# Performance work log

Hardware: AMD Instinct MI355X
Metric: run time of the kernel (lower is better)

The kernel has to match this reference:

```python
import jax, jax.numpy as jnp
import numpy as np

B, S, D, H = 4, 2048, 1024, 16
HD = D // H  # head_dim = 64


def setup_inputs() -> dict:
    key = jax.random.key(0)
    ks = jax.random.split(key, 9)
    sc = 1.0 / np.sqrt(D)
    return {
        "x": jax.random.normal(ks[0], (B, S, D), dtype=jnp.float32),
        "Wq": jax.random.normal(ks[1], (D, D), dtype=jnp.float32) * sc,
        "bq": jnp.zeros((D,), dtype=jnp.float32),
        "Wk": jax.random.normal(ks[2], (D, D), dtype=jnp.float32) * sc,
        "bk": jnp.zeros((D,), dtype=jnp.float32),
        "Wv": jax.random.normal(ks[3], (D, D), dtype=jnp.float32) * sc,
        "bv": jnp.zeros((D,), dtype=jnp.float32),
        "Wo": jax.random.normal(ks[4], (D, D), dtype=jnp.float32) * sc,
        "bo": jnp.zeros((D,), dtype=jnp.float32),
    }


def reference(x, Wq, bq, Wk, bk, Wv, bv, Wo, bo):
    # QKV projections (torch Linear: x @ W.T + b), reshape to [B, H, S, HD]
    def proj(W, b):
        return (x @ W.T + b).reshape(B, S, H, HD).transpose(0, 2, 1, 3)

    Q, K, V = proj(Wq, bq), proj(Wk, bk), proj(Wv, bv)
    scores = jnp.einsum("bhqd,bhkd->bhqk", Q, K) / jnp.sqrt(jnp.float32(HD))
    attn = jax.nn.softmax(scores, axis=-1)  # dropout is identity at eval
    ctx = jnp.einsum("bhqk,bhkd->bhqd", attn, V)
    ctx = ctx.transpose(0, 2, 1, 3).reshape(B, S, D)
    out = ctx @ Wo.T + bo
    return out, attn
```

## Files before the change

### kernel.cpp

```cpp
#include <hip/hip_runtime.h>
#include <stdint.h>

#define Mm 8192
#define Dd 1024

typedef unsigned short u16;
typedef __attribute__((ext_vector_type(8))) short bf16x8;
typedef __attribute__((ext_vector_type(4))) float f32x4;
typedef __attribute__((ext_vector_type(4))) u16 u16x4;

__device__ __forceinline__ u16 f2bf(float f) {
  union { float f; uint32_t u; } c; c.f = f;
  uint32_t u = c.u;
  return (u16)((u + 0x7fffu + ((u >> 16) & 1u)) >> 16);
}

__device__ __forceinline__ float EXP2(float x) {
#if __has_builtin(__builtin_amdgcn_exp2f)
  return __builtin_amdgcn_exp2f(x);
#else
  return exp2f(x);
#endif
}

__device__ __forceinline__ float LOG2(float x) {
#if __has_builtin(__builtin_amdgcn_logf)
  return __builtin_amdgcn_logf(x);
#else
  return log2f(x);
#endif
}

__device__ __forceinline__ uint32_t cvtpk(float a, float b) {
  uint32_t r;
  asm("v_cvt_pk_bf16_f32 %0, %1, %2" : "=v"(r) : "v"(a), "v"(b));
  return r;
}

__device__ __forceinline__ void gll16(const void* g, void* l) {
  __builtin_amdgcn_global_load_lds((const __attribute__((address_space(1))) void*)g,
                                   (__attribute__((address_space(3))) void*)l, 16, 0, 0);
}

__global__ void cvt_all(const float* __restrict__ x, const float* __restrict__ wq,
                        const float* __restrict__ wk, const float* __restrict__ wv,
                        const float* __restrict__ wo, u16* __restrict__ out) {
  const int xn4 = 2097152, wn4 = 262144;
  const int total = xn4 + 4 * wn4;
  int i = blockIdx.x * blockDim.x + threadIdx.x;
  int stride = gridDim.x * blockDim.x;
  for (; i < total; i += stride) {
    const float* src; int off;
    if (i < xn4) { src = x; off = i; }
    else {
      int j = i - xn4; int wsel = j >> 18; off = j & (wn4 - 1);
      src = (wsel == 0) ? wq : (wsel == 1) ? wk : (wsel == 2) ? wv : wo;
    }
    float4 v = ((const float4*)src)[off];
    u16x4 o;
    o.x = f2bf(v.x); o.y = f2bf(v.y); o.z = f2bf(v.z); o.w = f2bf(v.w);
    ((u16x4*)out)[i] = o;
  }
}

__global__ __launch_bounds__(256) void gemm_qkv(
    const u16* __restrict__ A, const u16* __restrict__ Wt,
    const float* __restrict__ bq, const float* __restrict__ bk, const float* __restrict__ bv,
    u16* __restrict__ Qo, u16* __restrict__ Ko, u16* __restrict__ Vo, float qscale)
{
  __shared__ u16 As[128 * 32];
  __shared__ u16 Bs[128 * 32];
  const int K = 1024, tiles_n = 24;
  int nwg = 64 * 24;
  int bid = blockIdx.x;
  { int q = nwg >> 3; bid = (bid & 7) * q + (bid >> 3); }
  int tm = bid / tiles_n, tn = bid % tiles_n;
  int tid = threadIdx.x;
  int wid = tid >> 6, lane = tid & 63;
  int wr = wid >> 1, wc = wid & 1;

  f32x4 acc[4][4] = {};
  int a_row = wr * 64 + (lane & 15);
  int b_row = wc * 64 + (lane & 15);
  int frag_k = (lane >> 4) * 8;

  const u16* ga0 = A + (size_t)(tm * 128 + wid * 32 + (lane >> 2)) * K + (lane & 3) * 8;
  const u16* ga1 = ga0 + (size_t)16 * K;
  const u16* gb0 = Wt + (size_t)(tn * 128 + wid * 32 + (lane >> 2)) * K + (lane & 3) * 8;
  const u16* gb1 = gb0 + (size_t)16 * K;
  u16* lA0 = As + wid * 1024;
  u16* lA1 = As + wid * 1024 + 512;
  u16* lB0 = Bs + wid * 1024;
  u16* lB1 = Bs + wid * 1024 + 512;

  for (int kt = 0; kt < K; kt += 32) {
    gll16(ga0 + kt, lA0);
    gll16(ga1 + kt, lA1);
    gll16(gb0 + kt, lB0);
    gll16(gb1 + kt, lB1);
    __syncthreads();
    bf16x8 af[4], bfr[4];
#pragma unroll
    for (int i = 0; i < 4; i++)
      af[i] = *(const bf16x8*)(As + (a_row + i * 16) * 32 + frag_k);
#pragma unroll
    for (int i = 0; i < 4; i++)
      bfr[i] = *(const bf16x8*)(Bs + (b_row + i * 16) * 32 + frag_k);
#pragma unroll
    for (int i = 0; i < 4; i++)
#pragma unroll
      for (int j = 0; j < 4; j++)
        acc[i][j] = __builtin_amdgcn_mfma_f32_16x16x32_bf16(af[i], bfr[j], acc[i][j], 0, 0, 0);
    __syncthreads();
  }

#pragma unroll
  for (int i = 0; i < 4; i++) {
#pragma unroll
    for (int j = 0; j < 4; j++) {
      int col = tn * 128 + wc * 64 + j * 16 + (lane & 15);
      int wsel = col >> 10, c10 = col & 1023;
      int h = c10 >> 6, hd = c10 & 63;
      float bvv = (wsel == 0 ? bq : wsel == 1 ? bk : bv)[c10];
      int row0 = tm * 128 + wr * 64 + i * 16 + (lane >> 4) * 4;
      int b_ = row0 >> 11, s0 = row0 & 2047;
      if (wsel == 2) {
        u16x4 o;
#pragma unroll
        for (int r = 0; r < 4; r++) o[r] = f2bf(acc[i][j][r] + bvv);
        *(u16x4*)&Vo[((size_t)(b_ * 16 + h) * 64 + hd) * 2048 + s0] = o;
      } else {
        u16* dst = (wsel == 0) ? Qo : Ko;
        float sc = (wsel == 0) ? qscale : 1.0f;
#pragma unroll
        for (int r = 0; r < 4; r++)
          dst[(((size_t)(b_ * 16 + h) * 2048 + (s0 + r)) << 6) + hd] = f2bf((acc[i][j][r] + bvv) * sc);
      }
    }
  }
}

__global__ __launch_bounds__(256) void gemm_out(
    const u16* __restrict__ A, const u16* __restrict__ Bt,
    const float* __restrict__ bias, float* __restrict__ out,
    int M, int N, int K)
{
  __shared__ u16 As[128 * 32];
  __shared__ u16 Bs[128 * 32];
  int tiles_n = N >> 7;
  int nwg = (M >> 7) * tiles_n;
  int bid = blockIdx.x;
  { int q = nwg >> 3; bid = (bid & 7) * q + (bid >> 3); }
  int tm = bid / tiles_n, tn = bid % tiles_n;
  int tid = threadIdx.x;
  int wid = tid >> 6, lane = tid & 63;
  int wr = wid >> 1, wc = wid & 1;

  f32x4 acc[4][4] = {};
  int a_row = wr * 64 + (lane & 15);
  int b_row = wc * 64 + (lane & 15);
  int frag_k = (lane >> 4) * 8;

  const u16* ga0 = A + (size_t)(tm * 128 + wid * 32 + (lane >> 2)) * K + (lane & 3) * 8;
  const u16* ga1 = ga0 + (size_t)16 * K;
  const u16* gb0 = Bt + (size_t)(tn * 128 + wid * 32 + (lane >> 2)) * K + (lane & 3) * 8;
  const u16* gb1 = gb0 + (size_t)16 * K;
  u16* lA0 = As + wid * 1024;
  u16* lA1 = As + wid * 1024 + 512;
  u16* lB0 = Bs + wid * 1024;
  u16* lB1 = Bs + wid * 1024 + 512;

  for (int kt = 0; kt < K; kt += 32) {
    gll16(ga0 + kt, lA0);
    gll16(ga1 + kt, lA1);
    gll16(gb0 + kt, lB0);
    gll16(gb1 + kt, lB1);
    __syncthreads();
    bf16x8 af[4], bfr[4];
#pragma unroll
    for (int i = 0; i < 4; i++)
      af[i] = *(const bf16x8*)(As + (a_row + i * 16) * 32 + frag_k);
#pragma unroll
    for (int i = 0; i < 4; i++)
      bfr[i] = *(const bf16x8*)(Bs + (b_row + i * 16) * 32 + frag_k);
#pragma unroll
    for (int i = 0; i < 4; i++)
#pragma unroll
      for (int j = 0; j < 4; j++)
        acc[i][j] = __builtin_amdgcn_mfma_f32_16x16x32_bf16(af[i], bfr[j], acc[i][j], 0, 0, 0);
    __syncthreads();
  }

#pragma unroll
  for (int i = 0; i < 4; i++)
#pragma unroll
    for (int j = 0; j < 4; j++) {
      int col = tn * 128 + wc * 64 + j * 16 + (lane & 15);
      float bv = bias[col];
#pragma unroll
      for (int r = 0; r < 4; r++) {
        int row = tm * 128 + wr * 64 + i * 16 + (lane >> 4) * 4 + r;
        out[(size_t)row * N + col] = acc[i][j][r] + bv;
      }
    }
}

__global__ __launch_bounds__(512, 4) void attn_fused2(
    const u16* __restrict__ Qb, const u16* __restrict__ Kb,
    const u16* __restrict__ Vtb, float* __restrict__ attn_out,
    u16* __restrict__ ctxb)
{
  __shared__ u16 Ks[4][4096];
  __shared__ u16 Vs[4][4096];
  __shared__ u16 Ps[8192];

  int bid = blockIdx.x;
  int swz = (bid & 7) * 64 + (bid >> 3);
  int bh = swz >> 3, qtb = swz & 7;
  int tid = threadIdx.x, w = tid >> 6, lane = tid & 63;
  int g = lane >> 4, l15 = lane & 15;

  const u16* Kg = Kb + (size_t)bh * 2048 * 64;
  const u16* Vg = Vtb + (size_t)bh * 64 * 2048;
  const u16* Qg0 = Qb + ((size_t)bh * 2048 + qtb * 256) * 64;
  const u16* Qg1 = Qg0 + (size_t)128 * 64;
  float* Ag0 = attn_out + ((size_t)bh * 2048 + qtb * 256) * 2048;
  float* Ag1 = Ag0 + (size_t)128 * 2048;

  int qloc = w * 16 + l15;
  bf16x8 aqA0 = *(const bf16x8*)(Qg0 + (size_t)qloc * 64 + g * 8);
  bf16x8 aqA1 = *(const bf16x8*)(Qg0 + (size_t)qloc * 64 + 32 + g * 8);
  bf16x8 aqB0 = *(const bf16x8*)(Qg1 + (size_t)qloc * 64 + g * 8);
  bf16x8 aqB1 = *(const bf16x8*)(Qg1 + (size_t)qloc * 64 + 32 + g * 8);

  int srow = w * 8 + (lane >> 3);
  int schunk = (lane & 7) ^ (lane >> 3);
  const u16* Ksrc = Kg + (size_t)srow * 64 + schunk * 8;
  const u16* Vsrc = Vg + (size_t)srow * 2048 + schunk * 8;

  int xq = (qloc & 7) << 4;
  char* Pb = (char*)Ps + qloc * 128;
  int b_ = bh >> 4, h = bh & 15;

  float ls0 = 0.f, ls1 = 0.f, ls2 = 0.f, ls3 = 0.f;
#pragma unroll
  for (int p = 0; p < 3; p++)
    gll16(Ksrc + (size_t)p * 4096, (char*)Ks[p] + w * 1024);
  for (int it = 0; it < 32; ++it) {
    if (it < 29) gll16(Ksrc + (size_t)(it + 3) * 4096, (char*)Ks[(it + 3) & 3] + w * 1024);
    if (it < 29)      asm volatile("s_waitcnt vmcnt(3)" ::: "memory");
    else if (it == 29) asm volatile("s_waitcnt vmcnt(2)" ::: "memory");
    else if (it == 30) asm volatile("s_waitcnt vmcnt(1)" ::: "memory");
    else               asm volatile("s_waitcnt vmcnt(0)" ::: "memory");
    __builtin_amdgcn_s_barrier();
    f32x4 s[4] = {};
    const char* Kbase = (const char*)Ks[it & 3];
    __builtin_amdgcn_s_setprio(1);
#pragma unroll
    for (int t = 0; t < 4; t++) {
      int kr = t * 16 + l15;
      int x = (kr & 7) << 4;
      bf16x8 k0 = *(const bf16x8*)(Kbase + kr * 128 + ((g * 16) ^ x));
      bf16x8 k1 = *(const bf16x8*)(Kbase + kr * 128 + ((64 + g * 16) ^ x));
      s[t] = __builtin_amdgcn_mfma_f32_16x16x32_bf16(k0, aqA0, s[t], 0, 0, 0);
      s[t] = __builtin_amdgcn_mfma_f32_16x16x32_bf16(k1, aqA1, s[t], 0, 0, 0);
    }
    __builtin_amdgcn_s_setprio(0);
#pragma unroll
    for (int r = 0; r < 4; r++) {
      ls0 += EXP2(s[0][r]); ls1 += EXP2(s[1][r]);
      ls2 += EXP2(s[2][r]); ls3 += EXP2(s[3][r]);
    }
    asm volatile("" ::: "memory");
    __builtin_amdgcn_s_barrier();
  }
  float lsum = (ls0 + ls1) + (ls2 + ls3);
  lsum += __shfl_xor(lsum, 16);
  lsum += __shfl_xor(lsum, 32);
  float lrA = -LOG2(lsum);

  f32x4 ctx[4] = {};
  float lb0 = 0.f, lb1 = 0.f, lb2 = 0.f, lb3 = 0.f;
  asm volatile("s_waitcnt vmcnt(0)" ::: "memory");
  __builtin_amdgcn_s_barrier();
#pragma unroll
  for (int p = 0; p < 3; p++) {
    gll16(Ksrc + (size_t)p * 4096, (char*)Ks[p] + w * 1024);
    gll16(Vsrc + (size_t)p * 64,  (char*)Vs[p] + w * 1024);
  }
  for (int it = 0; it < 32; ++it) {
    if (it < 29) {
      gll16(Ksrc + (size_t)(it + 3) * 4096, (char*)Ks[(it + 3) & 3] + w * 1024);
      gll16(Vsrc + (size_t)(it + 3) * 64,  (char*)Vs[(it + 3) & 3] + w * 1024);
    }
    if (it == 0)      asm volatile("s_waitcnt vmcnt(6)" ::: "memory");
    else if (it == 1) asm volatile("s_waitcnt vmcnt(22)" ::: "memory");
    else if (it == 2) asm volatile("s_waitcnt vmcnt(38)" ::: "memory");
    else if (it < 29) asm volatile("s_waitcnt vmcnt(54)" ::: "memory");
    else              asm volatile("s_waitcnt vmcnt(32)" ::: "memory");
    __builtin_amdgcn_s_barrier();
    f32x4 s[4] = {};
    const char* Kbase = (const char*)Ks[it & 3];
    __builtin_amdgcn_s_setprio(1);
#pragma unroll
    for (int t = 0; t < 4; t++) {
      int kr = t * 16 + l15;
      int x = (kr & 7) << 4;
      bf16x8 k0 = *(const bf16x8*)(Kbase + kr * 128 + ((g * 16) ^ x));
      bf16x8 k1 = *(const bf16x8*)(Kbase + kr * 128 + ((64 + g * 16) ^ x));
      s[t] = __builtin_amdgcn_mfma_f32_16x16x32_bf16(k0, aqA0, s[t], 0, 0, 0);
      s[t] = __builtin_amdgcn_mfma_f32_16x16x32_bf16(k1, aqA1, s[t], 0, 0, 0);
    }
    __builtin_amdgcn_s_setprio(0);
    float* Arow = Ag0 + (size_t)qloc * 2048 + it * 64 + g * 4;
#pragma unroll
    for (int t = 0; t < 4; t++) {
      f32x4 p;
#pragma unroll
      for (int r = 0; r < 4; r++) p[r] = EXP2(s[t][r] + lrA);
      __builtin_nontemporal_store(p, (f32x4*)(Arow + t * 16));
      uint2 pk;
      pk.x = cvtpk(p[0], p[1]);
      pk.y = cvtpk(p[2], p[3]);
      *(uint2*)(Pb + ((t * 32 + g * 8) ^ xq)) = pk;
    }
    __builtin_amdgcn_s_setprio(1);
#pragma unroll
    for (int kk = 0; kk < 2; kk++) {
      bf16x8 ap = *(const bf16x8*)(Pb + ((kk * 64 + g * 16) ^ xq));
#pragma unroll
      for (int t = 0; t < 4; t++) {
        int dr = t * 16 + l15;
        bf16x8 bv = *(const bf16x8*)((const char*)Vs[it & 3] + dr * 128 + ((kk * 64 + g * 16) ^ ((dr & 7) << 4)));
        ctx[t] = __builtin_amdgcn_mfma_f32_16x16x32_bf16(ap, bv, ctx[t], 0, 0, 0);
      }
    }
    f32x4 sb[4] = {};
#pragma unroll
    for (int t = 0; t < 4; t++) {
      int kr = t * 16 + l15;
      int x = (kr & 7) << 4;
      bf16x8 k0 = *(const bf16x8*)(Kbase + kr * 128 + ((g * 16) ^ x));
      bf16x8 k1 = *(const bf16x8*)(Kbase + kr * 128 + ((64 + g * 16) ^ x));
      sb[t] = __builtin_amdgcn_mfma_f32_16x16x32_bf16(k0, aqB0, sb[t], 0, 0, 0);
      sb[t] = __builtin_amdgcn_mfma_f32_16x16x32_bf16(k1, aqB1, sb[t], 0, 0, 0);
    }
    __builtin_amdgcn_s_setprio(0);
#pragma unroll
    for (int r = 0; r < 4; r++) {
      lb0 += EXP2(sb[0][r]); lb1 += EXP2(sb[1][r]);
      lb2 += EXP2(sb[2][r]); lb3 += EXP2(sb[3][r]);
    }
    asm volatile("" ::: "memory");
    __builtin_amdgcn_s_barrier();
  }
  float lsb = (lb0 + lb1) + (lb2 + lb3);
  lsb += __shfl_xor(lsb, 16);
  lsb += __shfl_xor(lsb, 32);
  float lrB = -LOG2(lsb);

#pragma unroll
  for (int t = 0; t < 4; t++)
#pragma unroll
    for (int r = 0; r < 4; r++) {
      int qg = qtb * 256 + w * 16 + g * 4 + r;
      int col = h * 64 + t * 16 + l15;
      ctxb[((size_t)b_ * 2048 + qg) * 1024 + col] = f2bf(ctx[t][r]);
    }

  f32x4 ctxB[4] = {};
  asm volatile("s_waitcnt vmcnt(0)" ::: "memory");
  __builtin_amdgcn_s_barrier();
#pragma unroll
  for (int p = 0; p < 3; p++) {
    gll16(Ksrc + (size_t)p * 4096, (char*)Ks[p] + w * 1024);
    gll16(Vsrc + (size_t)p * 64,  (char*)Vs[p] + w * 1024);
  }
  for (int it = 0; it < 32; ++it) {
    if (it < 29) {
      gll16(Ksrc + (size_t)(it + 3) * 4096, (char*)Ks[(it + 3) & 3] + w * 1024);
      gll16(Vsrc + (size_t)(it + 3) * 64,  (char*)Vs[(it + 3) & 3] + w * 1024);
    }
    if (it == 0)      asm volatile("s_waitcnt vmcnt(6)" ::: "memory");
    else if (it == 1) asm volatile("s_waitcnt vmcnt(22)" ::: "memory");
    else if (it == 2) asm volatile("s_waitcnt vmcnt(38)" ::: "memory");
    else if (it < 29) asm volatile("s_waitcnt vmcnt(54)" ::: "memory");
    else              asm volatile("s_waitcnt vmcnt(32)" ::: "memory");
    __builtin_amdgcn_s_barrier();
    f32x4 s[4] = {};
    const char* Kbase = (const char*)Ks[it & 3];
    __builtin_amdgcn_s_setprio(1);
#pragma unroll
    for (int t = 0; t < 4; t++) {
      int kr = t * 16 + l15;
      int x = (kr & 7) << 4;
      bf16x8 k0 = *(const bf16x8*)(Kbase + kr * 128 + ((g * 16) ^ x));
      bf16x8 k1 = *(const bf16x8*)(Kbase + kr * 128 + ((64 + g * 16) ^ x));
      s[t] = __builtin_amdgcn_mfma_f32_16x16x32_bf16(k0, aqB0, s[t], 0, 0, 0);
      s[t] = __builtin_amdgcn_mfma_f32_16x16x32_bf16(k1, aqB1, s[t], 0, 0, 0);
    }
    __builtin_amdgcn_s_setprio(0);
    float* Arow = Ag1 + (size_t)qloc * 2048 + it * 64 + g * 4;
#pragma unroll
    for (int t = 0; t < 4; t++) {
      f32x4 p;
#pragma unroll
      for (int r = 0; r < 4; r++) p[r] = EXP2(s[t][r] + lrB);
      __builtin_nontemporal_store(p, (f32x4*)(Arow + t * 16));
      uint2 pk;
      pk.x = cvtpk(p[0], p[1]);
      pk.y = cvtpk(p[2], p[3]);
      *(uint2*)(Pb + ((t * 32 + g * 8) ^ xq)) = pk;
    }
    __builtin_amdgcn_s_setprio(1);
#pragma unroll
    for (int kk = 0; kk < 2; kk++) {
      bf16x8 ap = *(const bf16x8*)(Pb + ((kk * 64 + g * 16) ^ xq));
#pragma unroll
      for (int t = 0; t < 4; t++) {
        int dr = t * 16 + l15;
        bf16x8 bv = *(const bf16x8*)((const char*)Vs[it & 3] + dr * 128 + ((kk * 64 + g * 16) ^ ((dr & 7) << 4)));
        ctxB[t] = __builtin_amdgcn_mfma_f32_16x16x32_bf16(ap, bv, ctxB[t], 0, 0, 0);
      }
    }
    __builtin_amdgcn_s_setprio(0);
    asm volatile("" ::: "memory");
    __builtin_amdgcn_s_barrier();
  }

#pragma unroll
  for (int t = 0; t < 4; t++)
#pragma unroll
    for (int r = 0; r < 4; r++) {
      int qg = qtb * 256 + 128 + w * 16 + g * 4 + r;
      int col = h * 64 + t * 16 + l15;
      ctxb[((size_t)b_ * 2048 + qg) * 1024 + col] = f2bf(ctxB[t][r]);
    }
}

extern "C" void kernel_launch(void* const* d_in, const int* in_sizes, int n_in,
                              void* d_out, int out_size, void* d_ws, size_t ws_size,
                              hipStream_t stream) {
  const float* x  = (const float*)d_in[0];
  const float* Wq = (const float*)d_in[1];
  const float* bq = (const float*)d_in[2];
  const float* Wk = (const float*)d_in[3];
  const float* bk = (const float*)d_in[4];
  const float* Wv = (const float*)d_in[5];
  const float* bv = (const float*)d_in[6];
  const float* Wo = (const float*)d_in[7];
  const float* bo = (const float*)d_in[8];

  u16* xb   = (u16*)d_ws;
  u16* Wqb  = xb + (size_t)Mm * Dd;
  u16* Wkb  = Wqb + (size_t)Dd * Dd;
  u16* Wvb  = Wkb + (size_t)Dd * Dd;
  u16* Wob  = Wvb + (size_t)Dd * Dd;
  u16* Qb   = Wob + (size_t)Dd * Dd;
  u16* Kbuf = Qb + (size_t)Mm * Dd;
  u16* Vtb  = Kbuf + (size_t)Mm * Dd;
  u16* ctxb = Vtb + (size_t)Mm * Dd;

  float* out_f = (float*)d_out;
  float* attn_o = out_f + (size_t)Mm * Dd;

  cvt_all<<<2048, 256, 0, stream>>>(x, Wq, Wk, Wv, Wo, xb);

  const float qscale = 0.125f * 1.44269504088896340736f;
  gemm_qkv<<<1536, 256, 0, stream>>>(xb, Wqb, bq, bk, bv, Qb, Kbuf, Vtb, qscale);
  attn_fused2<<<512, 512, 0, stream>>>(Qb, Kbuf, Vtb, attn_o, ctxb);
  gemm_out<<<512, 256, 0, stream>>>(ctxb, Wob, bo, out_f, Mm, Dd, Dd);
}
```

Before: 532.0 us.

## Switch attention to 32x32 MFMA with register-resident P via permlane swap

Rewrites the fused attention kernel around 32x32x16 bf16 MFMAs so each wave owns 32 query rows instead of two 16-row halves handled in separate passes. The probabilities are converted to bf16 and rearranged across lanes with v_permlane32_swap rather than round-tripping through shared memory, which removes the P scratch buffer. The aim is fewer K/V reloads, fewer passes and less LDS traffic. In exchange each lane holds more accumulator registers, the vmcnt wait counts are retuned, and the lane-layout assumptions must be exactly right.

After: 1.099 ms. 107% more time.

```diff
diff --git a/kernel.cpp b/kernel.cpp
--- a/kernel.cpp
+++ b/kernel.cpp
@@ -7,6 +7,7 @@
 typedef unsigned short u16;
 typedef __attribute__((ext_vector_type(8))) short bf16x8;
 typedef __attribute__((ext_vector_type(4))) float f32x4;
+typedef __attribute__((ext_vector_type(16))) float f32x16;
 typedef __attribute__((ext_vector_type(4))) u16 u16x4;
 
 __device__ __forceinline__ u16 f2bf(float f) {
@@ -205,84 +206,73 @@
     }
 }
 
-__global__ __launch_bounds__(512, 4) void attn_fused2(
+__global__ __launch_bounds__(512, 4) void attn_fused32(
     const u16* __restrict__ Qb, const u16* __restrict__ Kb,
     const u16* __restrict__ Vtb, float* __restrict__ attn_out,
     u16* __restrict__ ctxb)
 {
   __shared__ u16 Ks[4][4096];
   __shared__ u16 Vs[4][4096];
-  __shared__ u16 Ps[8192];
 
   int bid = blockIdx.x;
   int swz = (bid & 7) * 64 + (bid >> 3);
   int bh = swz >> 3, qtb = swz & 7;
   int tid = threadIdx.x, w = tid >> 6, lane = tid & 63;
-  int g = lane >> 4, l15 = lane & 15;
+  int l31 = lane & 31, hi = lane >> 5;
 
   const u16* Kg = Kb + (size_t)bh * 2048 * 64;
   const u16* Vg = Vtb + (size_t)bh * 64 * 2048;
-  const u16* Qg0 = Qb + ((size_t)bh * 2048 + qtb * 256) * 64;
-  const u16* Qg1 = Qg0 + (size_t)128 * 64;
-  float* Ag0 = attn_out + ((size_t)bh * 2048 + qtb * 256) * 2048;
-  float* Ag1 = Ag0 + (size_t)128 * 2048;
-
-  int qloc = w * 16 + l15;
-  bf16x8 aqA0 = *(const bf16x8*)(Qg0 + (size_t)qloc * 64 + g * 8);
-  bf16x8 aqA1 = *(const bf16x8*)(Qg0 + (size_t)qloc * 64 + 32 + g * 8);
-  bf16x8 aqB0 = *(const bf16x8*)(Qg1 + (size_t)qloc * 64 + g * 8);
-  bf16x8 aqB1 = *(const bf16x8*)(Qg1 + (size_t)qloc * 64 + 32 + g * 8);
+  const u16* Qg = Qb + ((size_t)bh * 2048 + qtb * 256) * 64;
+  float* Ag = attn_out + ((size_t)bh * 2048 + qtb * 256) * 2048;
+
+  int qloc = w * 32 + l31;
+  bf16x8 aq[4];
+#pragma unroll
+  for (int m = 0; m < 4; m++)
+    aq[m] = *(const bf16x8*)(Qg + (size_t)qloc * 64 + m * 16 + hi * 8);
 
   int srow = w * 8 + (lane >> 3);
   int schunk = (lane & 7) ^ (lane >> 3);
   const u16* Ksrc = Kg + (size_t)srow * 64 + schunk * 8;
   const u16* Vsrc = Vg + (size_t)srow * 2048 + schunk * 8;
 
-  int xq = (qloc & 7) << 4;
-  char* Pb = (char*)Ps + qloc * 128;
-  int b_ = bh >> 4, h = bh & 15;
-
-  float ls0 = 0.f, ls1 = 0.f, ls2 = 0.f, ls3 = 0.f;
+  int xsw = (l31 & 7) << 4;
+
+  float e0 = 0.f, e1 = 0.f, e2 = 0.f, e3 = 0.f;
 #pragma unroll
   for (int p = 0; p < 3; p++)
     gll16(Ksrc + (size_t)p * 4096, (char*)Ks[p] + w * 1024);
   for (int it = 0; it < 32; ++it) {
     if (it < 29) gll16(Ksrc + (size_t)(it + 3) * 4096, (char*)Ks[(it + 3) & 3] + w * 1024);
-    if (it < 29)      asm volatile("s_waitcnt vmcnt(3)" ::: "memory");
+    if (it < 29)       asm volatile("s_waitcnt vmcnt(3)" ::: "memory");
     else if (it == 29) asm volatile("s_waitcnt vmcnt(2)" ::: "memory");
     else if (it == 30) asm volatile("s_waitcnt vmcnt(1)" ::: "memory");
     else               asm volatile("s_waitcnt vmcnt(0)" ::: "memory");
     __builtin_amdgcn_s_barrier();
-    f32x4 s[4] = {};
     const char* Kbase = (const char*)Ks[it & 3];
+    f32x16 s0 = {}, s1 = {};
     __builtin_amdgcn_s_setprio(1);
 #pragma unroll
-    for (int t = 0; t < 4; t++) {
-      int kr = t * 16 + l15;
-      int x = (kr & 7) << 4;
-      bf16x8 k0 = *(const bf16x8*)(Kbase + kr * 128 + ((g * 16) ^ x));
-      bf16x8 k1 = *(const bf16x8*)(Kbase + kr * 128 + ((64 + g * 16) ^ x));
-      s[t] = __builtin_amdgcn_mfma_f32_16x16x32_bf16(k0, aqA0, s[t], 0, 0, 0);
-      s[t] = __builtin_amdgcn_mfma_f32_16x16x32_bf16(k1, aqA1, s[t], 0, 0, 0);
+    for (int m = 0; m < 4; m++) {
+      bf16x8 k0 = *(const bf16x8*)(Kbase + l31 * 128 + ((m * 32 + hi * 16) ^ xsw));
+      bf16x8 k1 = *(const bf16x8*)(Kbase + (32 + l31) * 128 + ((m * 32 + hi * 16) ^ xsw));
+      s0 = __builtin_amdgcn_mfma_f32_32x32x16_bf16(k0, aq[m], s0, 0, 0, 0);
+      s1 = __builtin_amdgcn_mfma_f32_32x32x16_bf16(k1, aq[m], s1, 0, 0, 0);
     }
     __builtin_amdgcn_s_setprio(0);
 #pragma unroll
-    for (int r = 0; r < 4; r++) {
-      ls0 += EXP2(s[0][r]); ls1 += EXP2(s[1][r]);
-      ls2 += EXP2(s[2][r]); ls3 += EXP2(s[3][r]);
+    for (int r = 0; r < 8; r++) {
+      e0 += EXP2(s0[2 * r]); e1 += EXP2(s0[2 * r + 1]);
+      e2 += EXP2(s1[2 * r]); e3 += EXP2(s1[2 * r + 1]);
     }
     asm volatile("" ::: "memory");
     __builtin_amdgcn_s_barrier();
   }
-  float lsum = (ls0 + ls1) + (ls2 + ls3);
-  lsum += __shfl_xor(lsum, 16);
+  float lsum = (e0 + e1) + (e2 + e3);
   lsum += __shfl_xor(lsum, 32);
-  float lrA = -LOG2(lsum);
-
-  f32x4 ctx[4] = {};
-  float lb0 = 0.f, lb1 = 0.f, lb2 = 0.f, lb3 = 0.f;
-  asm volatile("s_waitcnt vmcnt(0)" ::: "memory");
-  __builtin_amdgcn_s_barrier();
+  float lr2 = -LOG2(lsum);
+
+  f32x16 c0 = {}, c1 = {};
 #pragma unroll
   for (int p = 0; p < 3; p++) {
     gll16(Ksrc + (size_t)p * 4096, (char*)Ks[p] + w * 1024);
@@ -294,148 +284,75 @@
       gll16(Vsrc + (size_t)(it + 3) * 64,  (char*)Vs[(it + 3) & 3] + w * 1024);
     }
     if (it == 0)      asm volatile("s_waitcnt vmcnt(6)" ::: "memory");
-    else if (it == 1) asm volatile("s_waitcnt vmcnt(22)" ::: "memory");
-    else if (it == 2) asm volatile("s_waitcnt vmcnt(38)" ::: "memory");
-    else if (it < 29) asm volatile("s_waitcnt vmcnt(54)" ::: "memory");
-    else              asm volatile("s_waitcnt vmcnt(32)" ::: "memory");
+    else if (it == 1) asm volatile("s_waitcnt vmcnt(14)" ::: "memory");
+    else if (it == 2) asm volatile("s_waitcnt vmcnt(22)" ::: "memory");
+    else if (it < 29) asm volatile("s_waitcnt vmcnt(30)" ::: "memory");
+    else              asm volatile("s_waitcnt vmcnt(24)" ::: "memory");
     __builtin_amdgcn_s_barrier();
-    f32x4 s[4] = {};
     const char* Kbase = (const char*)Ks[it & 3];
+    const char* Vbase = (const char*)Vs[it & 3];
+    f32x16 s0 = {}, s1 = {};
     __builtin_amdgcn_s_setprio(1);
 #pragma unroll
-    for (int t = 0; t < 4; t++) {
-      int kr = t * 16 + l15;
-      int x = (kr & 7) << 4;
-      bf16x8 k0 = *(const bf16x8*)(Kbase + kr * 128 + ((g * 16) ^ x));
-      bf16x8 k1 = *(const bf16x8*)(Kbase + kr * 128 + ((64 + g * 16) ^ x));
-      s[t] = __builtin_amdgcn_mfma_f32_16x16x32_bf16(k0, aqA0, s[t], 0, 0, 0);
-      s[t] = __builtin_amdgcn_mfma_f32_16x16x32_bf16(k1, aqA1, s[t], 0, 0, 0);
+    for (int m = 0; m < 4; m++) {
+      bf16x8 k0 = *(const bf16x8*)(Kbase + l31 * 128 + ((m * 32 + hi * 16) ^ xsw));
+      bf16x8 k1 = *(const bf16x8*)(Kbase + (32 + l31) * 128 + ((m * 32 + hi * 16) ^ xsw));
+      s0 = __builtin_amdgcn_mfma_f32_32x32x16_bf16(k0, aq[m], s0, 0, 0, 0);
+      s1 = __builtin_amdgcn_mfma_f32_32x32x16_bf16(k1, aq[m], s1, 0, 0, 0);
     }
     __builtin_amdgcn_s_setprio(0);
-    float* Arow = Ag0 + (size_t)qloc * 2048 + it * 64 + g * 4;
-#pragma unroll
-    for (int t = 0; t < 4; t++) {
-      f32x4 p;
-#pragma unroll
-      for (int r = 0; r < 4; r++) p[r] = EXP2(s[t][r] + lrA);
-      __builtin_nontemporal_store(p, (f32x4*)(Arow + t * 16));
-      uint2 pk;
-      pk.x = cvtpk(p[0], p[1]);
-      pk.y = cvtpk(p[2], p[3]);
-      *(uint2*)(Pb + ((t * 32 + g * 8) ^ xq)) = pk;
-    }
+
+    float* Arow = Ag + (size_t)qloc * 2048 + it * 64;
+    uint32_t fr[4][4];
+#pragma unroll
+    for (int kb = 0; kb < 2; kb++) {
+      float pv[16];
+#pragma unroll
+      for (int r = 0; r < 16; r++) pv[r] = EXP2((kb ? s1[r] : s0[r]) + lr2);
+#pragma unroll
+      for (int q4 = 0; q4 < 4; q4++) {
+        f32x4 st = { pv[q4 * 4], pv[q4 * 4 + 1], pv[q4 * 4 + 2], pv[q4 * 4 + 3] };
+        __builtin_nontemporal_store(st, (f32x4*)(Arow + kb * 32 + q4 * 8 + hi * 4));
+      }
+      uint32_t a  = cvtpk(pv[0], pv[1]),   a2 = cvtpk(pv[2], pv[3]);
+      uint32_t b  = cvtpk(pv[4], pv[5]),   b2 = cvtpk(pv[6], pv[7]);
+      asm("v_permlane32_swap_b32 %0, %1" : "+v"(a), "+v"(b));
+      asm("v_permlane32_swap_b32 %0, %1" : "+v"(a2), "+v"(b2));
+      fr[kb * 2][0] = a; fr[kb * 2][1] = a2; fr[kb * 2][2] = b; fr[kb * 2][3] = b2;
+      a  = cvtpk(pv[8], pv[9]);   a2 = cvtpk(pv[10], pv[11]);
+      b  = cvtpk(pv[12], pv[13]); b2 = cvtpk(pv[14], pv[15]);
+      asm("v_permlane32_swap_b32 %0, %1" : "+v"(a), "+v"(b));
+      asm("v_permlane32_swap_b32 %0, %1" : "+v"(a2), "+v"(b2));
+      fr[kb * 2 + 1][0] = a; fr[kb * 2 + 1][1] = a2; fr[kb * 2 + 1][2] = b; fr[kb * 2 + 1][3] = b2;
+    }
+
     __builtin_amdgcn_s_setprio(1);
 #pragma unroll
-    for (int kk = 0; kk < 2; kk++) {
-      bf16x8 ap = *(const bf16x8*)(Pb + ((kk * 64 + g * 16) ^ xq));
-#pragma unroll
-      for (int t = 0; t < 4; t++) {
-        int dr = t * 16 + l15;
-        bf16x8 bv = *(const bf16x8*)((const char*)Vs[it & 3] + dr * 128 + ((kk * 64 + g * 16) ^ ((dr & 7) << 4)));
-        ctx[t] = __builtin_amdgcn_mfma_f32_16x16x32_bf16(ap, bv, ctx[t], 0, 0, 0);
-      }
-    }
-    f32x4 sb[4] = {};
-#pragma unroll
-    for (int t = 0; t < 4; t++) {
-      int kr = t * 16 + l15;
-      int x = (kr & 7) << 4;
-      bf16x8 k0 = *(const bf16x8*)(Kbase + kr * 128 + ((g * 16) ^ x));
-      bf16x8 k1 = *(const bf16x8*)(Kbase + kr * 128 + ((64 + g * 16) ^ x));
-      sb[t] = __builtin_amdgcn_mfma_f32_16x16x32_bf16(k0, aqB0, sb[t], 0, 0, 0);
-      sb[t] = __builtin_amdgcn_mfma_f32_16x16x32_bf16(k1, aqB1, sb[t], 0, 0, 0);
-    }
-    __builtin_amdgcn_s_setprio(0);
-#pragma unroll
-    for (int r = 0; r < 4; r++) {
-      lb0 += EXP2(sb[0][r]); lb1 += EXP2(sb[1][r]);
-      lb2 += EXP2(sb[2][r]); lb3 += EXP2(sb[3][r]);
-    }
-    asm volatile("" ::: "memory");
-    __builtin_amdgcn_s_barrier();
-  }
-  float lsb = (lb0 + lb1) + (lb2 + lb3);
-  lsb += __shfl_xor(lsb, 16);
-  lsb += __shfl_xor(lsb, 32);
-  float lrB = -LOG2(lsb);
-
-#pragma unroll
-  for (int t = 0; t < 4; t++)
-#pragma unroll
-    for (int r = 0; r < 4; r++) {
-      int qg = qtb * 256 + w * 16 + g * 4 + r;
-      int col = h * 64 + t * 16 + l15;
-      ctxb[((size_t)b_ * 2048 + qg) * 1024 + col] = f2bf(ctx[t][r]);
-    }
-
-  f32x4 ctxB[4] = {};
-  asm volatile("s_waitcnt vmcnt(0)" ::: "memory");
-  __builtin_amdgcn_s_barrier();
-#pragma unroll
-  for (int p = 0; p < 3; p++) {
-    gll16(Ksrc + (size_t)p * 4096, (char*)Ks[p] + w * 1024);
-    gll16(Vsrc + (size_t)p * 64,  (char*)Vs[p] + w * 1024);
-  }
-  for (int it = 0; it < 32; ++it) {
-    if (it < 29) {
-      gll16(Ksrc + (size_t)(it + 3) * 4096, (char*)Ks[(it + 3) & 3] + w * 1024);
-      gll16(Vsrc + (size_t)(it + 3) * 64,  (char*)Vs[(it + 3) & 3] + w * 1024);
-    }
-    if (it == 0)      asm volatile("s_waitcnt vmcnt(6)" ::: "memory");
-    else if (it == 1) asm volatile("s_waitcnt vmcnt(22)" ::: "memory");
-    else if (it == 2) asm volatile("s_waitcnt vmcnt(38)" ::: "memory");
-    else if (it < 29) asm volatile("s_waitcnt vmcnt(54)" ::: "memory");
-    else              asm volatile("s_waitcnt vmcnt(32)" ::: "memory");
-    __builtin_amdgcn_s_barrier();
-    f32x4 s[4] = {};
-    const char* Kbase = (const char*)Ks[it & 3];
-    __builtin_amdgcn_s_setprio(1);
-#pragma unroll
-    for (int t = 0; t < 4; t++) {
-      int kr = t * 16 + l15;
-      int x = (kr & 7) << 4;
-      bf16x8 k0 = *(const bf16x8*)(Kbase + kr * 128 + ((g * 16) ^ x));
-      bf16x8 k1 = *(const bf16x8*)(Kbase + kr * 128 + ((64 + g * 16) ^ x));
-      s[t] = __builtin_amdgcn_mfma_f32_16x16x32_bf16(k0, aqB0, s[t], 0, 0, 0);
-      s[t] = __builtin_amdgcn_mfma_f32_16x16x32_bf16(k1, aqB1, s[t], 0, 0, 0);
-    }
-    __builtin_amdgcn_s_setprio(0);
-    float* Arow = Ag1 + (size_t)qloc * 2048 + it * 64 + g * 4;
-#pragma unroll
-    for (int t = 0; t < 4; t++) {
-      f32x4 p;
-#pragma unroll
-      for (int r = 0; r < 4; r++) p[r] = EXP2(s[t][r] + lrB);
-      __builtin_nontemporal_store(p, (f32x4*)(Arow + t * 16));
-      uint2 pk;
-      pk.x = cvtpk(p[0], p[1]);
-      pk.y = cvtpk(p[2], p[3]);
-      *(uint2*)(Pb + ((t * 32 + g * 8) ^ xq)) = pk;
-    }
-    __builtin_amdgcn_s_setprio(1);
-#pragma unroll
-    for (int kk = 0; kk < 2; kk++) {
-      bf16x8 ap = *(const bf16x8*)(Pb + ((kk * 64 + g * 16) ^ xq));
-#pragma unroll
-      for (int t = 0; t < 4; t++) {
-        int dr = t * 16 + l15;
-        bf16x8 bv = *(const bf16x8*)((const char*)Vs[it & 3] + dr * 128 + ((kk * 64 + g * 16) ^ ((dr & 7) << 4)));
-        ctxB[t] = __builtin_amdgcn_mfma_f32_16x16x32_bf16(ap, bv, ctxB[t], 0, 0, 0);
-      }
+    for (int m = 0; m < 4; m++) {
+      union { uint32_t u[4]; bf16x8 v; } pc;
+      pc.u[0] = fr[m][0]; pc.u[1] = fr[m][1]; pc.u[2] = fr[m][2]; pc.u[3] = fr[m][3];
+      bf16x8 v0 = *(const bf16x8*)(Vbase + l31 * 128 + ((m * 32 + hi * 16) ^ xsw));
+      bf16x8 v1 = *(const bf16x8*)(Vbase + (32 + l31) * 128 + ((m * 32 + hi * 16) ^ xsw));
+      c0 = __builtin_amdgcn_mfma_f32_32x32x16_bf16(v0, pc.v, c0, 0, 0, 0);
+      c1 = __builtin_amdgcn_mfma_f32_32x32x16_bf16(v1, pc.v, c1, 0, 0, 0);
     }
     __builtin_amdgcn_s_setprio(0);
     asm volatile("" ::: "memory");
     __builtin_amdgcn_s_barrier();
   }
 
-#pragma unroll
-  for (int t = 0; t < 4; t++)
-#pragma unroll
-    for (int r = 0; r < 4; r++) {
-      int qg = qtb * 256 + 128 + w * 16 + g * 4 + r;
-      int col = h * 64 + t * 16 + l15;
-      ctxb[((size_t)b_ * 2048 + qg) * 1024 + col] = f2bf(ctxB[t][r]);
-    }
+  int b_ = bh >> 4, h = bh & 15;
+  u16* crow = ctxb + ((size_t)b_ * 2048 + qtb * 256 + qloc) * 1024 + h * 64;
+#pragma unroll
+  for (int q4 = 0; q4 < 4; q4++) {
+    uint2 o;
+    o.x = cvtpk(c0[q4 * 4], c0[q4 * 4 + 1]);
+    o.y = cvtpk(c0[q4 * 4 + 2], c0[q4 * 4 + 3]);
+    *(uint2*)(crow + q4 * 8 + hi * 4) = o;
+    o.x = cvtpk(c1[q4 * 4], c1[q4 * 4 + 1]);
+    o.y = cvtpk(c1[q4 * 4 + 2], c1[q4 * 4 + 3]);
+    *(uint2*)(crow + 32 + q4 * 8 + hi * 4) = o;
+  }
 }
 
 extern "C" void kernel_launch(void* const* d_in, const int* in_sizes, int n_in,
@@ -468,6 +385,6 @@
 
   const float qscale = 0.125f * 1.44269504088896340736f;
   gemm_qkv<<<1536, 256, 0, stream>>>(xb, Wqb, bq, bk, bv, Qb, Kbuf, Vtb, qscale);
-  attn_fused2<<<512, 512, 0, stream>>>(Qb, Kbuf, Vtb, attn_o, ctxb);
+  attn_fused32<<<512, 512, 0, stream>>>(Qb, Kbuf, Vtb, attn_o, ctxb);
   gemm_out<<<512, 256, 0, stream>>>(ctxb, Wob, bo, out_f, Mm, Dd, Dd);
 }
```

## Process both query halves together in each K/V pass of fused attention

Applied to the files above, without the earlier changes.

The attention kernel previously ran three passes over K (and K/V): one pass for the first query half's sums, then a fused pass computing the first half's probabilities and context plus the second half's sums, then a third pass for the second half's context. It now computes sums for both 128-row query halves in one K pass, then does a single K/V pass that writes probabilities and context for both halves. This removes one full stream of K/V tiles through shared memory and its barriers, at the cost of more live accumulators (two sets of scores and contexts), which may raise register pressure under the 512-thread launch bound. The vmcnt wait counts are retuned to match the new load pattern.

Result: faster. 495.0 us (-6.9%).

```diff
diff --git a/kernel.cpp b/kernel.cpp
--- a/kernel.cpp
+++ b/kernel.cpp
@@ -205,7 +205,7 @@
     }
 }
 
-__global__ __launch_bounds__(512, 4) void attn_fused2(
+__global__ __launch_bounds__(512, 4) void attn_fused16q2(
     const u16* __restrict__ Qb, const u16* __restrict__ Kb,
     const u16* __restrict__ Vtb, float* __restrict__ attn_out,
     u16* __restrict__ ctxb)
@@ -222,16 +222,14 @@
 
   const u16* Kg = Kb + (size_t)bh * 2048 * 64;
   const u16* Vg = Vtb + (size_t)bh * 64 * 2048;
-  const u16* Qg0 = Qb + ((size_t)bh * 2048 + qtb * 256) * 64;
-  const u16* Qg1 = Qg0 + (size_t)128 * 64;
-  float* Ag0 = attn_out + ((size_t)bh * 2048 + qtb * 256) * 2048;
-  float* Ag1 = Ag0 + (size_t)128 * 2048;
+  const u16* Qg = Qb + ((size_t)bh * 2048 + qtb * 256) * 64;
+  float* Ag = attn_out + ((size_t)bh * 2048 + qtb * 256) * 2048;
 
   int qloc = w * 16 + l15;
-  bf16x8 aqA0 = *(const bf16x8*)(Qg0 + (size_t)qloc * 64 + g * 8);
-  bf16x8 aqA1 = *(const bf16x8*)(Qg0 + (size_t)qloc * 64 + 32 + g * 8);
-  bf16x8 aqB0 = *(const bf16x8*)(Qg1 + (size_t)qloc * 64 + g * 8);
-  bf16x8 aqB1 = *(const bf16x8*)(Qg1 + (size_t)qloc * 64 + 32 + g * 8);
+  bf16x8 aqA0 = *(const bf16x8*)(Qg + (size_t)qloc * 64 + g * 8);
+  bf16x8 aqA1 = *(const bf16x8*)(Qg + (size_t)qloc * 64 + 32 + g * 8);
+  bf16x8 aqB0 = *(const bf16x8*)(Qg + (size_t)(128 + qloc) * 64 + g * 8);
+  bf16x8 aqB1 = *(const bf16x8*)(Qg + (size_t)(128 + qloc) * 64 + 32 + g * 8);
 
   int srow = w * 8 + (lane >> 3);
   int schunk = (lane & 7) ^ (lane >> 3);
@@ -240,21 +238,20 @@
 
   int xq = (qloc & 7) << 4;
   char* Pb = (char*)Ps + qloc * 128;
-  int b_ = bh >> 4, h = bh & 15;
-
-  float ls0 = 0.f, ls1 = 0.f, ls2 = 0.f, ls3 = 0.f;
+
+  float eA0 = 0.f, eA1 = 0.f, eB0 = 0.f, eB1 = 0.f;
 #pragma unroll
   for (int p = 0; p < 3; p++)
     gll16(Ksrc + (size_t)p * 4096, (char*)Ks[p] + w * 1024);
   for (int it = 0; it < 32; ++it) {
     if (it < 29) gll16(Ksrc + (size_t)(it + 3) * 4096, (char*)Ks[(it + 3) & 3] + w * 1024);
-    if (it < 29)      asm volatile("s_waitcnt vmcnt(3)" ::: "memory");
+    if (it < 29)       asm volatile("s_waitcnt vmcnt(3)" ::: "memory");
     else if (it == 29) asm volatile("s_waitcnt vmcnt(2)" ::: "memory");
     else if (it == 30) asm volatile("s_waitcnt vmcnt(1)" ::: "memory");
     else               asm volatile("s_waitcnt vmcnt(0)" ::: "memory");
     __builtin_amdgcn_s_barrier();
-    f32x4 s[4] = {};
     const char* Kbase = (const char*)Ks[it & 3];
+    f32x4 sA[4] = {}, sB[4] = {};
     __builtin_amdgcn_s_setprio(1);
 #pragma unroll
     for (int t = 0; t < 4; t++) {
@@ -262,27 +259,28 @@
       int x = (kr & 7) << 4;
       bf16x8 k0 = *(const bf16x8*)(Kbase + kr * 128 + ((g * 16) ^ x));
       bf16x8 k1 = *(const bf16x8*)(Kbase + kr * 128 + ((64 + g * 16) ^ x));
-      s[t] = __builtin_amdgcn_mfma_f32_16x16x32_bf16(k0, aqA0, s[t], 0, 0, 0);
-      s[t] = __builtin_amdgcn_mfma_f32_16x16x32_bf16(k1, aqA1, s[t], 0, 0, 0);
+      sA[t] = __builtin_amdgcn_mfma_f32_16x16x32_bf16(k0, aqA0, sA[t], 0, 0, 0);
+      sA[t] = __builtin_amdgcn_mfma_f32_16x16x32_bf16(k1, aqA1, sA[t], 0, 0, 0);
+      sB[t] = __builtin_amdgcn_mfma_f32_16x16x32_bf16(k0, aqB0, sB[t], 0, 0, 0);
+      sB[t] = __builtin_amdgcn_mfma_f32_16x16x32_bf16(k1, aqB1, sB[t], 0, 0, 0);
     }
     __builtin_amdgcn_s_setprio(0);
 #pragma unroll
-    for (int r = 0; r < 4; r++) {
-      ls0 += EXP2(s[0][r]); ls1 += EXP2(s[1][r]);
-      ls2 += EXP2(s[2][r]); ls3 += EXP2(s[3][r]);
-    }
+    for (int t = 0; t < 4; t++)
+#pragma unroll
+      for (int r = 0; r < 4; r++) {
+        if (t & 1) { eA1 += EXP2(sA[t][r]); eB1 += EXP2(sB[t][r]); }
+        else       { eA0 += EXP2(sA[t][r]); eB0 += EXP2(sB[t][r]); }
+      }
     asm volatile("" ::: "memory");
     __builtin_amdgcn_s_barrier();
   }
-  float lsum = (ls0 + ls1) + (ls2 + ls3);
-  lsum += __shfl_xor(lsum, 16);
-  lsum += __shfl_xor(lsum, 32);
-  float lrA = -LOG2(lsum);
-
-  f32x4 ctx[4] = {};
-  float lb0 = 0.f, lb1 = 0.f, lb2 = 0.f, lb3 = 0.f;
-  asm volatile("s_waitcnt vmcnt(0)" ::: "memory");
-  __builtin_amdgcn_s_barrier();
+  float lsA = eA0 + eA1, lsB = eB0 + eB1;
+  lsA += __shfl_xor(lsA, 16); lsA += __shfl_xor(lsA, 32);
+  lsB += __shfl_xor(lsB, 16); lsB += __shfl_xor(lsB, 32);
+  float lrA = -LOG2(lsA), lrB = -LOG2(lsB);
+
+  f32x4 cA[4] = {}, cB[4] = {};
 #pragma unroll
   for (int p = 0; p < 3; p++) {
     gll16(Ksrc + (size_t)p * 4096, (char*)Ks[p] + w * 1024);
@@ -294,13 +292,16 @@
       gll16(Vsrc + (size_t)(it + 3) * 64,  (char*)Vs[(it + 3) & 3] + w * 1024);
     }
     if (it == 0)      asm volatile("s_waitcnt vmcnt(6)" ::: "memory");
-    else if (it == 1) asm volatile("s_waitcnt vmcnt(22)" ::: "memory");
-    else if (it == 2) asm volatile("s_waitcnt vmcnt(38)" ::: "memory");
-    else if (it < 29) asm volatile("s_waitcnt vmcnt(54)" ::: "memory");
-    else              asm volatile("s_waitcnt vmcnt(32)" ::: "memory");
+    else if (it == 1) asm volatile("s_waitcnt vmcnt(14)" ::: "memory");
+    else if (it == 2) asm volatile("s_waitcnt vmcnt(22)" ::: "memory");
+    else if (it < 29) asm volatile("s_waitcnt vmcnt(30)" ::: "memory");
+    else if (it == 29) asm volatile("s_waitcnt vmcnt(28)" ::: "memory");
+    else if (it == 30) asm volatile("s_waitcnt vmcnt(26)" ::: "memory");
+    else               asm volatile("s_waitcnt vmcnt(24)" ::: "memory");
     __builtin_amdgcn_s_barrier();
-    f32x4 s[4] = {};
     const char* Kbase = (const char*)Ks[it & 3];
+    const char* Vbase = (const char*)Vs[it & 3];
+    f32x4 sA[4] = {}, sB[4] = {};
     __builtin_amdgcn_s_setprio(1);
 #pragma unroll
     for (int t = 0; t < 4; t++) {
@@ -308,133 +309,78 @@
       int x = (kr & 7) << 4;
       bf16x8 k0 = *(const bf16x8*)(Kbase + kr * 128 + ((g * 16) ^ x));
       bf16x8 k1 = *(const bf16x8*)(Kbase + kr * 128 + ((64 + g * 16) ^ x));
-      s[t] = __builtin_amdgcn_mfma_f32_16x16x32_bf16(k0, aqA0, s[t], 0, 0, 0);
-      s[t] = __builtin_amdgcn_mfma_f32_16x16x32_bf16(k1, aqA1, s[t], 0, 0, 0);
+      sA[t] = __builtin_amdgcn_mfma_f32_16x16x32_bf16(k0, aqA0, sA[t], 0, 0, 0);
+      sA[t] = __builtin_amdgcn_mfma_f32_16x16x32_bf16(k1, aqA1, sA[t], 0, 0, 0);
+      sB[t] = __builtin_amdgcn_mfma_f32_16x16x32_bf16(k0, aqB0, sB[t], 0, 0, 0);
+      sB[t] = __builtin_amdgcn_mfma_f32_16x16x32_bf16(k1, aqB1, sB[t], 0, 0, 0);
     }
     __builtin_amdgcn_s_setprio(0);
-    float* Arow = Ag0 + (size_t)qloc * 2048 + it * 64 + g * 4;
-#pragma unroll
-    for (int t = 0; t < 4; t++) {
-      f32x4 p;
-#pragma unroll
-      for (int r = 0; r < 4; r++) p[r] = EXP2(s[t][r] + lrA);
-      __builtin_nontemporal_store(p, (f32x4*)(Arow + t * 16));
-      uint2 pk;
-      pk.x = cvtpk(p[0], p[1]);
-      pk.y = cvtpk(p[2], p[3]);
-      *(uint2*)(Pb + ((t * 32 + g * 8) ^ xq)) = pk;
-    }
-    __builtin_amdgcn_s_setprio(1);
-#pragma unroll
-    for (int kk = 0; kk < 2; kk++) {
-      bf16x8 ap = *(const bf16x8*)(Pb + ((kk * 64 + g * 16) ^ xq));
+
+    {
+      float* Arow = Ag + (size_t)qloc * 2048 + it * 64 + g * 4;
 #pragma unroll
       for (int t = 0; t < 4; t++) {
-        int dr = t * 16 + l15;
-        bf16x8 bv = *(const bf16x8*)((const char*)Vs[it & 3] + dr * 128 + ((kk * 64 + g * 16) ^ ((dr & 7) << 4)));
-        ctx[t] = __builtin_amdgcn_mfma_f32_16x16x32_bf16(ap, bv, ctx[t], 0, 0, 0);
-      }
-    }
-    f32x4 sb[4] = {};
-#pragma unroll
-    for (int t = 0; t < 4; t++) {
-      int kr = t * 16 + l15;
-      int x = (kr & 7) << 4;
-      bf16x8 k0 = *(const bf16x8*)(Kbase + kr * 128 + ((g * 16) ^ x));
-      bf16x8 k1 = *(const bf16x8*)(Kbase + kr * 128 + ((64 + g * 16) ^ x));
-      sb[t] = __builtin_amdgcn_mfma_f32_16x16x32_bf16(k0, aqB0, sb[t], 0, 0, 0);
-      sb[t] = __builtin_amdgcn_mfma_f32_16x16x32_bf16(k1, aqB1, sb[t], 0, 0, 0);
-    }
-    __builtin_amdgcn_s_setprio(0);
-#pragma unroll
-    for (int r = 0; r < 4; r++) {
-      lb0 += EXP2(sb[0][r]); lb1 += EXP2(sb[1][r]);
-      lb2 += EXP2(sb[2][r]); lb3 += EXP2(sb[3][r]);
+        f32x4 p;
+#pragma unroll
+        for (int r = 0; r < 4; r++) p[r] = EXP2(sA[t][r] + lrA);
+        __builtin_nontemporal_store(p, (f32x4*)(Arow + t * 16));
+        uint2 pk;
+        pk.x = cvtpk(p[0], p[1]);
+        pk.y = cvtpk(p[2], p[3]);
+        *(uint2*)(Pb + ((t * 32 + g * 8) ^ xq)) = pk;
+      }
+      __builtin_amdgcn_s_setprio(1);
+#pragma unroll
+      for (int kk = 0; kk < 2; kk++) {
+        bf16x8 ap = *(const bf16x8*)(Pb + ((kk * 64 + g * 16) ^ xq));
+#pragma unroll
+        for (int t = 0; t < 4; t++) {
+          int dr = t * 16 + l15;
+          bf16x8 bv = *(const bf16x8*)(Vbase + dr * 128 + ((kk * 64 + g * 16) ^ ((dr & 7) << 4)));
+          cA[t] = __builtin_amdgcn_mfma_f32_16x16x32_bf16(ap, bv, cA[t], 0, 0, 0);
+        }
+      }
+      __builtin_amdgcn_s_setprio(0);
+    }
+    {
+      float* Arow = Ag + (size_t)(128 + qloc) * 2048 + it * 64 + g * 4;
+#pragma unroll
+      for (int t = 0; t < 4; t++) {
+        f32x4 p;
+#pragma unroll
+        for (int r = 0; r < 4; r++) p[r] = EXP2(sB[t][r] + lrB);
+        __builtin_nontemporal_store(p, (f32x4*)(Arow + t * 16));
+        uint2 pk;
+        pk.x = cvtpk(p[0], p[1]);
+        pk.y = cvtpk(p[2], p[3]);
+        *(uint2*)(Pb + ((t * 32 + g * 8) ^ xq)) = pk;
+      }
+      __builtin_amdgcn_s_setprio(1);
+#pragma unroll
+      for (int kk = 0; kk < 2; kk++) {
+        bf16x8 ap = *(const bf16x8*)(Pb + ((kk * 64 + g * 16) ^ xq));
+#pragma unroll
+        for (int t = 0; t < 4; t++) {
+          int dr = t * 16 + l15;
+          bf16x8 bv = *(const bf16x8*)(Vbase + dr * 128 + ((kk * 64 + g * 16) ^ ((dr & 7) << 4)));
+          cB[t] = __builtin_amdgcn_mfma_f32_16x16x32_bf16(ap, bv, cB[t], 0, 0, 0);
+        }
+      }
+      __builtin_amdgcn_s_setprio(0);
     }
     asm volatile("" ::: "memory");
     __builtin_amdgcn_s_barrier();
   }
-  float lsb = (lb0 + lb1) + (lb2 + lb3);
-  lsb += __shfl_xor(lsb, 16);
-  lsb += __shfl_xor(lsb, 32);
-  float lrB = -LOG2(lsb);
-
+
+  int b_ = bh >> 4, h = bh & 15;
 #pragma unroll
   for (int t = 0; t < 4; t++)
 #pragma unroll
     for (int r = 0; r < 4; r++) {
-      int qg = qtb * 256 + w * 16 + g * 4 + r;
+      int qgA = qtb * 256 + w * 16 + g * 4 + r;
       int col = h * 64 + t * 16 + l15;
-      ctxb[((size_t)b_ * 2048 + qg) * 1024 + col] = f2bf(ctx[t][r]);
-    }
-
-  f32x4 ctxB[4] = {};
-  asm volatile("s_waitcnt vmcnt(0)" ::: "memory");
-  __builtin_amdgcn_s_barrier();
-#pragma unroll
-  for (int p = 0; p < 3; p++) {
-    gll16(Ksrc + (size_t)p * 4096, (char*)Ks[p] + w * 1024);
-    gll16(Vsrc + (size_t)p * 64,  (char*)Vs[p] + w * 1024);
-  }
-  for (int it = 0; it < 32; ++it) {
-    if (it < 29) {
-      gll16(Ksrc + (size_t)(it + 3) * 4096, (char*)Ks[(it + 3) & 3] + w * 1024);
-      gll16(Vsrc + (size_t)(it + 3) * 64,  (char*)Vs[(it + 3) & 3] + w * 1024);
-    }
-    if (it == 0)      asm volatile("s_waitcnt vmcnt(6)" ::: "memory");
-    else if (it == 1) asm volatile("s_waitcnt vmcnt(22)" ::: "memory");
-    else if (it == 2) asm volatile("s_waitcnt vmcnt(38)" ::: "memory");
-    else if (it < 29) asm volatile("s_waitcnt vmcnt(54)" ::: "memory");
-    else              asm volatile("s_waitcnt vmcnt(32)" ::: "memory");
-    __builtin_amdgcn_s_barrier();
-    f32x4 s[4] = {};
-    const char* Kbase = (const char*)Ks[it & 3];
-    __builtin_amdgcn_s_setprio(1);
-#pragma unroll
-    for (int t = 0; t < 4; t++) {
-      int kr = t * 16 + l15;
-      int x = (kr & 7) << 4;
-      bf16x8 k0 = *(const bf16x8*)(Kbase + kr * 128 + ((g * 16) ^ x));
-      bf16x8 k1 = *(const bf16x8*)(Kbase + kr * 128 + ((64 + g * 16) ^ x));
-      s[t] = __builtin_amdgcn_mfma_f32_16x16x32_bf16(k0, aqB0, s[t], 0, 0, 0);
-      s[t] = __builtin_amdgcn_mfma_f32_16x16x32_bf16(k1, aqB1, s[t], 0, 0, 0);
-    }
-    __builtin_amdgcn_s_setprio(0);
-    float* Arow = Ag1 + (size_t)qloc * 2048 + it * 64 + g * 4;
-#pragma unroll
-    for (int t = 0; t < 4; t++) {
-      f32x4 p;
-#pragma unroll
-      for (int r = 0; r < 4; r++) p[r] = EXP2(s[t][r] + lrB);
-      __builtin_nontemporal_store(p, (f32x4*)(Arow + t * 16));
-      uint2 pk;
-      pk.x = cvtpk(p[0], p[1]);
-      pk.y = cvtpk(p[2], p[3]);
-      *(uint2*)(Pb + ((t * 32 + g * 8) ^ xq)) = pk;
-    }
-    __builtin_amdgcn_s_setprio(1);
-#pragma unroll
-    for (int kk = 0; kk < 2; kk++) {
-      bf16x8 ap = *(const bf16x8*)(Pb + ((kk * 64 + g * 16) ^ xq));
-#pragma unroll
-      for (int t = 0; t < 4; t++) {
-        int dr = t * 16 + l15;
-        bf16x8 bv = *(const bf16x8*)((const char*)Vs[it & 3] + dr * 128 + ((kk * 64 + g * 16) ^ ((dr & 7) << 4)));
-        ctxB[t] = __builtin_amdgcn_mfma_f32_16x16x32_bf16(ap, bv, ctxB[t], 0, 0, 0);
-      }
-    }
-    __builtin_amdgcn_s_setprio(0);
-    asm volatile("" ::: "memory");
-    __builtin_amdgcn_s_barrier();
-  }
-
-#pragma unroll
-  for (int t = 0; t < 4; t++)
-#pragma unroll
-    for (int r = 0; r < 4; r++) {
-      int qg = qtb * 256 + 128 + w * 16 + g * 4 + r;
-      int col = h * 64 + t * 16 + l15;
-      ctxb[((size_t)b_ * 2048 + qg) * 1024 + col] = f2bf(ctxB[t][r]);
+      ctxb[((size_t)b_ * 2048 + qgA) * 1024 + col] = f2bf(cA[t][r]);
+      ctxb[((size_t)b_ * 2048 + qgA + 128) * 1024 + col] = f2bf(cB[t][r]);
     }
 }
 
@@ -468,6 +414,6 @@
 
   const float qscale = 0.125f * 1.44269504088896340736f;
   gemm_qkv<<<1536, 256, 0, stream>>>(xb, Wqb, bq, bk, bv, Qb, Kbuf, Vtb, qscale);
-  attn_fused2<<<512, 512, 0, stream>>>(Qb, Kbuf, Vtb, attn_o, ctxb);
+  attn_fused16q2<<<512, 512, 0, stream>>>(Qb, Kbuf, Vtb, attn_o, ctxb);
   gemm_out<<<512, 256, 0, stream>>>(ctxb, Wob, bo, out_f, Mm, Dd, Dd);
 }
```
